# Optimization experiments

Measured on AMD Instinct MI355X. Metric: run time of the kernel, lower is better.

## Reference

```python
import jax, jax.numpy as jnp
import numpy as np

N_DIM = 100_000      # n: primal variables
M_DIM = 200_000      # m: constraints
NNZ_A = 2_000_000    # nnz of A
NNZ_P_HALF = 250_000 # half of symmetric P nnz (mirrored)
CG_ITERS = 50


def _spmv(vals, rows, cols, v, nseg):
    # COO sparse matvec: out[r] += vals * v[cols]
    return jax.ops.segment_sum(vals * v[cols], rows, num_segments=nseg)


def setup_inputs() -> dict:
    key = jax.random.key(0)
    ks = jax.random.split(key, 16)
    n, m = N_DIM, M_DIM
    A_rows = jax.random.randint(ks[0], (NNZ_A,), 0, m, dtype=jnp.int32)
    A_cols = jax.random.randint(ks[1], (NNZ_A,), 0, n, dtype=jnp.int32)
    A_vals = jax.random.normal(ks[2], (NNZ_A,), jnp.float32) * 0.01
    # symmetric P via mirrored COO pattern
    pr = jax.random.randint(ks[3], (NNZ_P_HALF,), 0, n, dtype=jnp.int32)
    pc = jax.random.randint(ks[4], (NNZ_P_HALF,), 0, n, dtype=jnp.int32)
    pv = jax.random.normal(ks[5], (NNZ_P_HALF,), jnp.float32) * 0.01
    P_rows = jnp.concatenate([pr, pc])
    P_cols = jnp.concatenate([pc, pr])
    P_vals = jnp.concatenate([pv, pv])
    q = jax.random.normal(ks[6], (n,), jnp.float32)
    b = jax.random.normal(ks[7], (m,), jnp.float32)
    x = jax.random.normal(ks[8], (n,), jnp.float32)
    y = jnp.maximum(jax.random.normal(ks[9], (m,), jnp.float32), 0.0)
    s = jnp.maximum(jax.random.normal(ks[10], (m,), jnp.float32), 0.0)
    # data perturbations (dP shares P's symmetric pattern, dA shares A's pattern)
    dpv = jax.random.normal(ks[11], (NNZ_P_HALF,), jnp.float32) * 1e-3
    dP_vals = jnp.concatenate([dpv, dpv])
    dA_vals = jax.random.normal(ks[12], (NNZ_A,), jnp.float32) * 1e-3
    dq = jax.random.normal(ks[13], (n,), jnp.float32) * 1e-3
    db = jax.random.normal(ks[14], (m,), jnp.float32) * 1e-3
    return dict(P_rows=P_rows, P_cols=P_cols, P_vals=P_vals,
                A_rows=A_rows, A_cols=A_cols, A_vals=A_vals,
                q=q, b=b, x=x, y=y, s=s,
                dP_vals=dP_vals, dA_vals=dA_vals, dq=dq, db=db)


def reference(P_rows, P_cols, P_vals, A_rows, A_cols, A_vals,
              q, b, x, y, s, dP_vals, dA_vals, dq, db):
    n, m = q.shape[0], b.shape[0]
    Pmv = lambda v: _spmv(P_vals, P_rows, P_cols, v, n)
    Amv = lambda v: _spmv(A_vals, A_rows, A_cols, v, m)
    ATmv = lambda v: _spmv(A_vals, A_cols, A_rows, v, n)
    dPmv = lambda v: _spmv(dP_vals, P_rows, P_cols, v, n)
    dAmv = lambda v: _spmv(dA_vals, A_rows, A_cols, v, m)
    dATmv = lambda v: _spmv(dA_vals, A_cols, A_rows, v, n)

    # cone projection onto K* = R_+^m and its Jacobian (diagonal mask)
    v_ks = y - s
    mask = (v_ks > 0).astype(x.dtype)
    pi_m = jnp.maximum(v_ks, 0.0)     # pi_z = (x, Pi_{K*}(y-s), 1)
    tau = jnp.asarray(1.0, x.dtype)

    Px = Pmv(x)
    xTPx = x @ Px
    c3 = q + 2.0 * Px                  # d/dx of -x^T P x / tau at tau=1 -> -(q + 2Px)

    def Fmv(vv):
        # F = DzQ(pi_z) @ dPi - dPi + I
        vn, vm, vt = vv[:n], vv[n:n + m], vv[-1]
        un, um, ut = vn, mask * vm, vt          # dPi v
        r1 = Pmv(un) + ATmv(um) + q * ut        # [P, A^T, q]
        r2 = -Amv(un) + b * ut                  # [-A, 0, b]
        r3 = -(c3 @ un) - (b @ um) + xTPx * ut  # [-(q+2Px)^T, -b^T, x^TPx]
        return jnp.concatenate([r1 - un + vn, r2 - um + vm, (r3 - ut + vt)[None]])

    def FTmv(ww):
        # F^T = dPi @ (DzQ^T - I) + I   (dPi symmetric diagonal)
        wn, wm, wt = ww[:n], ww[n:n + m], ww[-1]
        t_n = Pmv(wn) - ATmv(wm) - c3 * wt
        t_m = Amv(wn) - b * wt
        t_t = (q @ wn) + (b @ wm) + xTPx * wt
        return jnp.concatenate([t_n, mask * (t_m - wm) + wm, t_t[None]])

    # d_data_Q applied at u = pi_z
    dd_n = dPmv(x) + dATmv(pi_m) + dq * tau
    dd_m = -dAmv(x) + db * tau
    dd_t = -(dq @ x) - (db @ pi_m) - (x @ dPmv(x)) / tau
    dd = jnp.concatenate([dd_n, dd_m, dd_t[None]])

    def solve_case():
        # least-squares solve of F dz = -dd via CG on normal equations (LSMR-equivalent solution)
        normal_op = lambda v: FTmv(Fmv(v))
        rhs = FTmv(-dd)
        dz, _ = jax.scipy.sparse.linalg.cg(normal_op, rhs, tol=1e-8, maxiter=CG_ITERS)
        return dz

    dz = jax.lax.cond(jnp.allclose(dd, 0.0), lambda: jnp.zeros_like(dd), solve_case)

    dzn, dzm, dzt = dz[:n], dz[n:n + m], dz[-1]
    dx = dzn - x * dzt
    t = mask * dzm                     # dPi_{K*}(v) @ dz_m
    dy = t - y * dzt
    ds = t - dzm - s * dzt
    return dx, dy, ds
```

## Files before the change

### kernel.cpp

```cpp
#include <hip/hip_runtime.h>

#define N_DIM 100000
#define M_DIM 200000
#define NNZ_A 2000000
#define NNZ_P 500000
#define NNZ_GN (NNZ_A + NNZ_P)
#define NMSUM 300000
#define NM1   300001
#define CG_ITERS 20
#define TPB 256
#define NSLOT 512
#define GOFF (20 * 5 * 64)
#define SETOFF (GOFF + 21 * 64)
#define REDSZ (SETOFF + 6 * 64)


__device__ __forceinline__ void blk_red_add(double v, double* dst) {
    __shared__ double sb[TPB];
    int tid = threadIdx.x;
    __syncthreads();
    sb[tid] = v;
    __syncthreads();
    for (int sh = TPB / 2; sh > 0; sh >>= 1) {
        if (tid < sh) sb[tid] += sb[tid + sh];
        __syncthreads();
    }
    if (tid == 0) atomicAdd(dst, sb[0]);
}

__device__ __forceinline__ void blk_red_add2(double v1, double v2, double* d1, double* d2) {
    __shared__ double sb1[TPB];
    __shared__ double sb2[TPB];
    int tid = threadIdx.x;
    __syncthreads();
    sb1[tid] = v1; sb2[tid] = v2;
    __syncthreads();
    for (int sh = TPB / 2; sh > 0; sh >>= 1) {
        if (tid < sh) { sb1[tid] += sb1[tid + sh]; sb2[tid] += sb2[tid + sh]; }
        __syncthreads();
    }
    if (tid == 0) { atomicAdd(d1, sb1[0]); atomicAdd(d2, sb2[0]); }
}

__device__ __forceinline__ double blk_sum64w(const double* src) {
    __shared__ double bsh;
    int t = threadIdx.x;
    if (t < 64) {
        double v = src[t];
        v += __shfl_xor(v, 32); v += __shfl_xor(v, 16); v += __shfl_xor(v, 8);
        v += __shfl_xor(v, 4);  v += __shfl_xor(v, 2);  v += __shfl_xor(v, 1);
        if (t == 0) bsh = v;
    }
    __syncthreads();
    double r = bsh;
    __syncthreads();
    return r;
}

__device__ __forceinline__ double row_dotx4(const int4* __restrict__ pp, int b2, int e2,
                                            const double* __restrict__ vin) {
    double s = 0.0;
    int k = b2;
    for (; k + 4 <= e2; k += 4) {
        int4 a = pp[k], b = pp[k + 1], c = pp[k + 2], d = pp[k + 3];
        double g0 = vin[a.x], g1 = vin[a.z], g2 = vin[b.x], g3 = vin[b.z];
        double g4 = vin[c.x], g5 = vin[c.z], g6 = vin[d.x], g7 = vin[d.z];
        s += (double)__int_as_float(a.y) * g0;
        s += (double)__int_as_float(a.w) * g1;
        s += (double)__int_as_float(b.y) * g2;
        s += (double)__int_as_float(b.w) * g3;
        s += (double)__int_as_float(c.y) * g4;
        s += (double)__int_as_float(c.w) * g5;
        s += (double)__int_as_float(d.y) * g6;
        s += (double)__int_as_float(d.w) * g7;
    }
    for (; k < e2; ++k) {
        int4 a = pp[k];
        s += (double)__int_as_float(a.y) * vin[a.x];
        s += (double)__int_as_float(a.w) * vin[a.z];
    }
    return s;
}

__device__ __forceinline__ double row_dotx4_half(const int4* __restrict__ pp, int b2, int e2,
                                                 const double* __restrict__ vin, int half) {
    int len = e2 - b2;
    int h1 = (len + 1) >> 1;
    int kb = b2 + (half ? h1 : 0);
    int ke = half ? e2 : (b2 + h1);
    double s = 0.0;
    int k = kb;
    for (; k + 4 <= ke; k += 4) {
        int4 a = pp[k], b = pp[k + 1], c = pp[k + 2], d = pp[k + 3];
        double g0 = vin[a.x], g1 = vin[a.z], g2 = vin[b.x], g3 = vin[b.z];
        double g4 = vin[c.x], g5 = vin[c.z], g6 = vin[d.x], g7 = vin[d.z];
        s += (double)__int_as_float(a.y) * g0;
        s += (double)__int_as_float(a.w) * g1;
        s += (double)__int_as_float(b.y) * g2;
        s += (double)__int_as_float(b.w) * g3;
        s += (double)__int_as_float(c.y) * g4;
        s += (double)__int_as_float(c.w) * g5;
        s += (double)__int_as_float(d.y) * g6;
        s += (double)__int_as_float(d.w) * g7;
    }
    for (; k + 2 <= ke; k += 2) {
        int4 a = pp[k], b = pp[k + 1];
        double g0 = vin[a.x], g1 = vin[a.z], g2 = vin[b.x], g3 = vin[b.z];
        s += (double)__int_as_float(a.y) * g0;
        s += (double)__int_as_float(a.w) * g1;
        s += (double)__int_as_float(b.y) * g2;
        s += (double)__int_as_float(b.w) * g3;
    }
    if (k < ke) {
        int4 a = pp[k];
        s += (double)__int_as_float(a.y) * vin[a.x];
        s += (double)__int_as_float(a.w) * vin[a.z];
    }
    s += __shfl_xor(s, 1);
    return s;
}

__device__ __forceinline__ double row_dot_d(const int2* __restrict__ pair,
                                            const float* __restrict__ dval, int beg, int end,
                                            const double* __restrict__ vin) {
    double s = 0.0;
    int k = beg;
    for (; k + 4 <= end; k += 4) {
        int c0 = pair[k].x, c1 = pair[k + 1].x, c2 = pair[k + 2].x, c3v = pair[k + 3].x;
        float d0 = dval[k], d1 = dval[k + 1], d2 = dval[k + 2], d3 = dval[k + 3];
        double g0 = vin[c0], g1 = vin[c1], g2 = vin[c2], g3 = vin[c3v];
        s += (double)d0 * g0;
        s += (double)d1 * g1;
        s += (double)d2 * g2;
        s += (double)d3 * g3;
    }
    for (; k < end; ++k)
        s += (double)dval[k] * vin[pair[k].x];
    return s;
}

__global__ __launch_bounds__(TPB) void k_init(double* sc, const float* y, const float* s,
                                              const float* x, double* mask_d, double* xpim,
                                              double* xcg, double* red,
                                              int* nP, int* cntGn, int* cntAr) {
    long i = (long)blockIdx.x * TPB + threadIdx.x;
    if (i < NSLOT) sc[i] = 0.0;
    if (i < REDSZ) red[i] = 0.0;
    if (i < M_DIM) {
        double v = (double)y[i] - (double)s[i];
        mask_d[i] = v > 0.0 ? 1.0 : 0.0;
        xpim[N_DIM + i] = v > 0.0 ? v : 0.0;
        cntAr[i] = 0;
    }
    if (i < N_DIM) {
        xpim[i] = (double)x[i];
        nP[i] = 0; cntGn[i] = 0;
    }
    if (i < NM1) xcg[i] = 0.0;
}

__global__ __launch_bounds__(TPB) void k_hist(const int* Ar, const int* Ac, const int* Pr,
                                              int* nP, int* cntGn, int* cntAr,
                                              int* seqP, int* seqGn, int* seqAr) {
    long k = (long)blockIdx.x * TPB + threadIdx.x;
    if (k < NNZ_A) {
        seqGn[k] = atomicAdd(&cntGn[Ac[k]], 1);
        seqAr[k] = atomicAdd(&cntAr[Ar[k]], 1);
    }
    if (k < NNZ_P) seqP[k] = atomicAdd(&nP[Pr[k]], 1);
}

__global__ __launch_bounds__(TPB) void k_comb(const int* nP, int* cntGn) {
    int i = blockIdx.x * TPB + threadIdx.x;
    if (i < N_DIM) cntGn[i] += nP[i];
}

__global__ __launch_bounds__(TPB) void k_scan1(const int* cnt, int len, int* exc, int* blksum) {
    __shared__ int sb[TPB];
    int i = blockIdx.x * TPB + threadIdx.x;
    int c = (i < len) ? cnt[i] : 0;
    int v = c + (c & 1);
    sb[threadIdx.x] = v;
    __syncthreads();
    for (int sh = 1; sh < TPB; sh <<= 1) {
        int t = (threadIdx.x >= sh) ? sb[threadIdx.x - sh] : 0;
        __syncthreads();
        sb[threadIdx.x] += t;
        __syncthreads();
    }
    if (i < len) exc[i] = sb[threadIdx.x] - v;
    if (threadIdx.x == TPB - 1) blksum[blockIdx.x] = sb[TPB - 1];
}

__global__ __launch_bounds__(1024) void k_scan2(int* blksum, int nb, int* total_out) {
    __shared__ int sb[1024];
    int t = threadIdx.x;
    int v = (t < nb) ? blksum[t] : 0;
    sb[t] = v;
    __syncthreads();
    for (int sh = 1; sh < 1024; sh <<= 1) {
        int x = (t >= sh) ? sb[t - sh] : 0;
        __syncthreads();
        sb[t] += x;
        __syncthreads();
    }
    if (t < nb) blksum[t] = sb[t] - v;
    if (t == nb - 1) *total_out = sb[t];
}

__global__ __launch_bounds__(TPB) void k_scan3(int* exc, const int* blksum, int len) {
    int i = blockIdx.x * TPB + threadIdx.x;
    if (i < len) exc[i] += blksum[blockIdx.x];
}

__global__ __launch_bounds__(TPB) void k_fillGn(const int* Pr, const int* Pc, const float* Pv,
                                                const float* dPv,
                                                const int* Ar, const int* Ac, const float* Av,
                                                const float* dAv,
                                                const int* rptrGn, const int* nP,
                                                const int* seqP, const int* seqGn,
                                                int2* pGn, float* dvalGn) {
    long k = (long)blockIdx.x * TPB + threadIdx.x;
    if (k < NNZ_P) {
        int r0 = Pr[k];
        int pos = rptrGn[r0] + seqP[k];
        pGn[pos] = make_int2(Pc[k], __float_as_int(Pv[k]));
        dvalGn[pos] = dPv[k];
    }
    if (k < NNZ_A) {
        int c0 = Ac[k];
        int pos = rptrGn[c0] + nP[c0] + seqGn[k];
        pGn[pos] = make_int2(N_DIM + Ar[k], __float_as_int(Av[k]));
        dvalGn[pos] = dAv[k];
    }
}
__global__ __launch_bounds__(TPB) void k_fillAr(const int* Ar, const int* Ac, const float* Av,
                                                const float* dAv, const int* rptrAr,
                                                const int* seqAr, int2* pAr, float* dvalAr) {
    long k = (long)blockIdx.x * TPB + threadIdx.x;
    if (k < NNZ_A) {
        int pos = rptrAr[Ar[k]] + seqAr[k];
        pAr[pos] = make_int2(Ac[k], __float_as_int(Av[k]));
        dvalAr[pos] = dAv[k];
    }
}

__global__ __launch_bounds__(TPB) void k_pad(const int* cntGn, const int* rptrGn,
                                             int2* pGn, float* dvalGn,
                                             const int* cntAr, const int* rptrAr,
                                             int2* pAr, float* dvalAr) {
    int i = blockIdx.x * TPB + threadIdx.x;
    if (i < N_DIM) {
        int c = cntGn[i];
        if (c & 1) { int pos = rptrGn[i] + c; pGn[pos] = make_int2(0, 0); dvalGn[pos] = 0.0f; }
    }
    if (i < M_DIM) {
        int c = cntAr[i];
        if (c & 1) { int pos = rptrAr[i] + c; pAr[pos] = make_int2(0, 0); dvalAr[pos] = 0.0f; }
    }
}

__global__ __launch_bounds__(TPB) void k_setup_n(const int* __restrict__ rptrGn,
                                                 const int2* __restrict__ pGn,
                                                 const float* __restrict__ dvalGn,
                                                 const int* __restrict__ nP,
                                                 const double* __restrict__ xpim,
                                                 const float* __restrict__ q,
                                                 const float* __restrict__ dq,
                                                 double* c3, double* dd, double* red) {
    int i = blockIdx.x * TPB + threadIdx.x;
    int slot = blockIdx.x & 63;
    double* S = red + SETOFF;
    double lx = 0.0, l1 = 0.0, l3 = 0.0;
    if (i < N_DIM) {
        int beg = rptrGn[i], end = rptrGn[i + 1];
        int np = nP[i];
        double px = 0.0, dpxv = 0.0, sa = 0.0;
        for (int k = beg; k < end; ++k) {
            int2 e = pGn[k];
            float dv = dvalGn[k];
            double g = xpim[e.x];
            if (k - beg < np) {
                px += (double)__int_as_float(e.y) * g;
                dpxv += (double)dv * g;
            } else {
                sa += (double)dv * g;
            }
        }
        c3[i] = (double)q[i] + 2.0 * px;
        dd[i] = dpxv + sa + (double)dq[i];
        double xi = xpim[i];
        lx = xi * px;
        l1 = (double)dq[i] * xi;
        l3 = xi * dpxv;
    }
    blk_red_add2(lx, l1, S + 0 * 64 + slot, S + 1 * 64 + slot);
    blk_red_add(l3, S + 3 * 64 + slot);
}

__global__ __launch_bounds__(TPB) void k_setup_m(const int* __restrict__ rptrAr,
                                                 const int2* __restrict__ pAr,
                                                 const float* __restrict__ dvalAr,
                                                 const double* __restrict__ xpim,
                                                 const float* __restrict__ db, double* dd,
                                                 double* red) {
    int j = blockIdx.x * TPB + threadIdx.x;
    int slot = blockIdx.x & 63;
    double* S = red + SETOFF;
    double l2 = 0.0;
    if (j < M_DIM) {
        double s = row_dot_d(pAr, dvalAr, rptrAr[j], rptrAr[j + 1], xpim);
        dd[N_DIM + j] = -s + (double)db[j];
        l2 = (double)db[j] * xpim[N_DIM + j];
    }
    blk_red_add(l2, S + 2 * 64 + slot);
}

__global__ __launch_bounds__(TPB) void k_negWC(double* dd, double* WC,
                                               const float* q, const float* b,
                                               double* red, double* sc) {
    long i = (long)blockIdx.x * TPB + threadIdx.x;
    int slot = blockIdx.x & 63;
    double* S = red + SETOFF;
    double l8 = 0.0, l9 = 0.0;
    if (i == NMSUM) {
        double xt = 0.0, s1 = 0.0, s2 = 0.0, s3 = 0.0;
        for (int k = 0; k < 64; ++k) {
            xt += S[k]; s1 += S[64 + k]; s2 += S[128 + k]; s3 += S[192 + k];
        }
        sc[0] = xt;
        dd[NMSUM] = s1 + s2 + s3;
    } else if (i < NM1) {
        double nv = -dd[i];
        dd[i] = nv;
        if (i < N_DIM) {
            WC[i] = nv;
            l8 = (double)q[i] * nv;
        } else {
            WC[i] = -nv;
            l9 = (double)b[i - N_DIM] * nv;
        }
    }
    blk_red_add2(l8, l9, S + 4 * 64 + slot, S + 5 * 64 + slot);
}

__global__ __launch_bounds__(TPB) void k_r(const int* __restrict__ rptrGn, const int2* __restrict__ pGn,
                                           const int* __restrict__ rptrAr, const int2* __restrict__ pAr,
                                           const double* __restrict__ WC, const double* __restrict__ c3,
                                           const double* __restrict__ mask_d, const float* __restrict__ b,
                                           const double* __restrict__ dd, double* r, double* p,
                                           double* red, const double* sc) {
    const int4* pGn4 = (const int4*)pGn;
    const int4* pAr4 = (const int4*)pAr;
    long i = (long)blockIdx.x * TPB + threadIdx.x;
    int slot = blockIdx.x & 63;
    double* S = red + SETOFF;
    double* gslot = red + GOFF;
    double rv = 0.0;
    bool wr = false;
    if (i < N_DIM) {
        double s = row_dotx4(pGn4, rptrGn[i] >> 1, rptrGn[i + 1] >> 1, WC);
        rv = s - c3[i] * dd[NMSUM];
        wr = true;
    } else if (i < NMSUM) {
        int j = (int)(i - N_DIM);
        double s = row_dotx4(pAr4, rptrAr[j] >> 1, rptrAr[j + 1] >> 1, WC);
        double wt = dd[NMSUM];
        double tmv = s - (double)b[j] * wt;
        double wm = dd[i];
        rv = mask_d[j] * (tmv - wm) + wm;
        wr = true;
    } else if (i == NMSUM) {
        double e1 = 0.0, e2 = 0.0;
        for (int k = 0; k < 64; ++k) { e1 += S[4 * 64 + k]; e2 += S[5 * 64 + k]; }
        rv = e1 + e2 + sc[0] * dd[NMSUM];
        wr = true;
    }
    double l = 0.0;
    if (wr) { r[i] = rv; p[i] = rv; l = rv * rv; }
    blk_red_add(l, gslot + slot);
}

__global__ __launch_bounds__(TPB) void k_iterA(const double* r, double* p,
                                               const double* mask_d, const double* c3,
                                               const float* b, double* pum,
                                               double* red, double* sc, int it) {
    double* ds = red + (long)it * 5 * 64;
    double* gslot = red + GOFF;
    double gn = blk_sum64w(gslot + (long)it * 64);
    if (blockIdx.x == 0 && threadIdx.x == 0) sc[64 + it] = gn;
    double beta = 0.0;
    if (it > 0) beta = gn / sc[64 + it - 1];
    long i = (long)blockIdx.x * TPB + threadIdx.x;
    int slot = blockIdx.x & 63;
    double l1 = 0.0, l2 = 0.0;
    if (i < NM1) {
        double pn;
        if (it > 0) {
            pn = r[i] + beta * p[i];
            p[i] = pn;
        } else {
            pn = p[i];
        }
        if (i < N_DIM) {
            l1 = c3[i] * pn;
            pum[i] = pn;
        } else if (i < NMSUM) {
            int j = (int)(i - N_DIM);
            double u = mask_d[j] * pn;
            pum[i] = u;
            l2 = (double)b[j] * u;
        }
    }
    blk_red_add2(l1, l2, ds + 0 * 64 + slot, ds + 1 * 64 + slot);
}

__global__ __launch_bounds__(TPB) void k_fmv(const int* __restrict__ rptrGn, const int2* __restrict__ pGn,
                                             const int* __restrict__ rptrAr, const int2* __restrict__ pAr,
                                             const float* __restrict__ q, const float* __restrict__ b,
                                             const double* __restrict__ p, const double* __restrict__ pum,
                                             double* __restrict__ Fpc, double* sc, double* red, int it) {
    const int4* pGn4 = (const int4*)pGn;
    const int4* pAr4 = (const int4*)pAr;
    double* ds = red + (long)it * 5 * 64;
    long t = (long)blockIdx.x * TPB + threadIdx.x;
    long i = t >> 1;
    int half = (int)(t & 1);
    int slot = blockIdx.x & 63;
    double ut = p[NMSUM];
    double l1 = 0.0, l2 = 0.0;
    if (i < N_DIM) {
        int ii = (int)i;
        double s = row_dotx4_half(pGn4, rptrGn[ii] >> 1, rptrGn[ii + 1] >> 1, pum, half);
        if (half == 0) {
            double r1 = s + (double)q[ii] * ut;
            double v = (r1 - p[i]) + p[i];
            Fpc[i] = v;
            l1 = (double)q[ii] * v;
        }
    } else if (i < NMSUM) {
        int j = (int)(i - N_DIM);
        double s = row_dotx4_half(pAr4, rptrAr[j] >> 1, rptrAr[j + 1] >> 1, pum, half);
        if (half == 0) {
            double r2 = -s + (double)b[j] * ut;
            double v = (r2 - pum[i]) + p[i];
            Fpc[i] = -v;
            l2 = (double)b[j] * v;
        }
    }
    blk_red_add2(l1, l2, ds + 2 * 64 + slot, ds + 3 * 64 + slot);
    if (blockIdx.x == gridDim.x - 1) {
        double d1 = blk_sum64w(ds + 0 * 64);
        double d2 = blk_sum64w(ds + 1 * 64);
        if (threadIdx.x == 0) {
            double r3 = -d1 - d2 + sc[0] * ut;
            sc[16 + it] = (r3 - ut) + ut;
        }
    }
}

__global__ __launch_bounds__(TPB) void k_ftmv(const int* __restrict__ rptrGn, const int2* __restrict__ pGn,
                                              const int* __restrict__ rptrAr, const int2* __restrict__ pAr,
                                              const float* __restrict__ b, const double* __restrict__ mask_d,
                                              const double* __restrict__ c3,
                                              const double* __restrict__ Fpc, const double* __restrict__ p,
                                              double* __restrict__ Ap, double* sc, double* red, int it) {
    const int4* pGn4 = (const int4*)pGn;
    const int4* pAr4 = (const int4*)pAr;
    double* ds = red + (long)it * 5 * 64;
    long t = (long)blockIdx.x * TPB + threadIdx.x;
    long i = t >> 1;
    int half = (int)(t & 1);
    int slot = blockIdx.x & 63;
    double wt = sc[16 + it];
    double l = 0.0;
    if (i < N_DIM) {
        int ii = (int)i;
        double s = row_dotx4_half(pGn4, rptrGn[ii] >> 1, rptrGn[ii + 1] >> 1, Fpc, half);
        if (half == 0) {
            double v = s - c3[ii] * wt;
            Ap[i] = v;
            l = p[i] * v;
        }
    } else if (i < NMSUM) {
        int j = (int)(i - N_DIM);
        double s = row_dotx4_half(pAr4, rptrAr[j] >> 1, rptrAr[j + 1] >> 1, Fpc, half);
        if (half == 0) {
            double tmv = s - (double)b[j] * wt;
            double wm = -Fpc[i];
            double v = mask_d[j] * (tmv - wm) + wm;
            Ap[i] = v;
            l = p[i] * v;
        }
    }
    blk_red_add(l, ds + 4 * 64 + slot);
    if (blockIdx.x == gridDim.x - 1) {
        double e1 = blk_sum64w(ds + 2 * 64);
        double e2 = blk_sum64w(ds + 3 * 64);
        if (threadIdx.x == 0) {
            double tt = e1 + e2 + sc[0] * wt;
            Ap[NMSUM] = tt;
            atomicAdd(ds + 4 * 64 + slot, p[NMSUM] * tt);
        }
    }
}

__global__ __launch_bounds__(TPB) void k_upd(const double* p, const double* Ap,
                                             double* xcg, double* r, double* red,
                                             const double* sc, int it) {
    double* ds = red + (long)it * 5 * 64;
    double* gslot = red + GOFF;
    double gcur = sc[64 + it];
    double pq = blk_sum64w(ds + 4 * 64);
    double alpha = gcur / pq;
    long i = (long)blockIdx.x * TPB + threadIdx.x;
    int slot = blockIdx.x & 63;
    double l = 0.0;
    if (i < NM1) {
        xcg[i] += alpha * p[i];
        double rn = r[i] - alpha * Ap[i];
        r[i] = rn;
        l = rn * rn;
    }
    blk_red_add(l, gslot + (long)(it + 1) * 64 + slot);
}

__global__ __launch_bounds__(TPB) void k_final(const double* xcg, const double* mask_d,
                                               const float* x, const float* y, const float* s,
                                               float* out) {
    int i = blockIdx.x * TPB + threadIdx.x;
    double dzt = xcg[NMSUM];
    if (i < N_DIM) {
        out[i] = (float)(xcg[i] - (double)x[i] * dzt);
    } else if (i < NMSUM) {
        int j = i - N_DIM;
        double dzm = xcg[N_DIM + j];
        double t = mask_d[j] * dzm;
        out[N_DIM + j] = (float)(t - (double)y[j] * dzt);
        out[N_DIM + M_DIM + j] = (float)(t - dzm - (double)s[j] * dzt);
    }
}

extern "C" void kernel_launch(void* const* d_in, const int* in_sizes, int n_in,
                              void* d_out, int out_size, void* d_ws, size_t ws_size,
                              hipStream_t stream) {
    const int*   Pr  = (const int*)d_in[0];
    const int*   Pc  = (const int*)d_in[1];
    const float* Pv  = (const float*)d_in[2];
    const int*   Ar  = (const int*)d_in[3];
    const int*   Ac  = (const int*)d_in[4];
    const float* Av  = (const float*)d_in[5];
    const float* q   = (const float*)d_in[6];
    const float* b   = (const float*)d_in[7];
    const float* x   = (const float*)d_in[8];
    const float* yv  = (const float*)d_in[9];
    const float* sv  = (const float*)d_in[10];
    const float* dPv = (const float*)d_in[11];
    const float* dAv = (const float*)d_in[12];
    const float* dq  = (const float*)d_in[13];
    const float* db  = (const float*)d_in[14];
    float* out = (float*)d_out;

    char* wp = (char*)d_ws;
    auto alloc = [&](size_t bytes) { char* r0 = wp; wp += (bytes + 255) & ~255ull; return r0; };

    double* sc     = (double*)alloc(NSLOT * 8);
    double* red    = (double*)alloc((size_t)REDSZ * 8);
    double* mask_d = (double*)alloc((size_t)M_DIM * 8);
    double* xpim   = (double*)alloc((size_t)NMSUM * 8);
    double* c3     = (double*)alloc((size_t)N_DIM * 8);
    double* dd     = (double*)alloc((size_t)NM1 * 8);
    double* r      = (double*)alloc((size_t)NM1 * 8);
    double* p      = (double*)alloc((size_t)NM1 * 8);
    double* xcg    = (double*)alloc((size_t)NM1 * 8);
    double* Ap     = (double*)alloc((size_t)NM1 * 8);
    double* pum    = (double*)alloc((size_t)NMSUM * 8);
    double* Fpc    = (double*)alloc((size_t)NMSUM * 8);
    double* WC     = (double*)alloc((size_t)NMSUM * 8);
    int2*  pGn    = (int2*)alloc(((size_t)NNZ_GN + N_DIM) * 8);
    int2*  pAr    = (int2*)alloc(((size_t)NNZ_A + M_DIM) * 8);
    float* dvalGn = (float*)alloc(((size_t)NNZ_GN + N_DIM) * 4);
    float* dvalAr = (float*)alloc(((size_t)NNZ_A + M_DIM) * 4);
    int*   rptrGn = (int*)alloc((size_t)(N_DIM + 1) * 4);
    int*   rptrAr = (int*)alloc((size_t)(M_DIM + 1) * 4);
    int*   nP     = (int*)alloc((size_t)N_DIM * 4);
    int*   cntGn  = (int*)alloc((size_t)N_DIM * 4);
    int*   cntAr  = (int*)alloc((size_t)M_DIM * 4);
    int*   seqP   = (int*)alloc((size_t)NNZ_P * 4);
    int*   seqGn  = (int*)alloc((size_t)NNZ_A * 4);
    int*   seqAr  = (int*)alloc((size_t)NNZ_A * 4);
    int*   blks   = (int*)alloc(1024 * 4);

    auto g = [](long n) { return dim3((unsigned)((n + TPB - 1) / TPB)); };
    dim3 gs((unsigned)((2L * NM1 + TPB - 1) / TPB + 1));

    hipLaunchKernelGGL(k_init, g(NM1), dim3(TPB), 0, stream, sc, yv, sv, x, mask_d, xpim, xcg, red,
                       nP, cntGn, cntAr);
    hipLaunchKernelGGL(k_hist, g(NNZ_A), dim3(TPB), 0, stream, Ar, Ac, Pr, nP, cntGn, cntAr,
                       seqP, seqGn, seqAr);
    hipLaunchKernelGGL(k_comb, g(N_DIM), dim3(TPB), 0, stream, nP, cntGn);

    auto scan = [&](int* cnt, int len, int* rptr) {
        int nb = (len + TPB - 1) / TPB;
        hipLaunchKernelGGL(k_scan1, dim3((unsigned)nb), dim3(TPB), 0, stream, cnt, len, rptr, blks);
        hipLaunchKernelGGL(k_scan2, dim3(1), dim3(1024), 0, stream, blks, nb, rptr + len);
        hipLaunchKernelGGL(k_scan3, dim3((unsigned)nb), dim3(TPB), 0, stream, rptr, blks, len);
    };
    scan(cntGn, N_DIM, rptrGn);
    scan(cntAr, M_DIM, rptrAr);

    hipLaunchKernelGGL(k_fillGn, g(NNZ_A), dim3(TPB), 0, stream, Pr, Pc, Pv, dPv,
                       Ar, Ac, Av, dAv, rptrGn, nP, seqP, seqGn, pGn, dvalGn);
    hipLaunchKernelGGL(k_fillAr, g(NNZ_A), dim3(TPB), 0, stream, Ar, Ac, Av, dAv,
                       rptrAr, seqAr, pAr, dvalAr);
    hipLaunchKernelGGL(k_pad, g(M_DIM), dim3(TPB), 0, stream, cntGn, rptrGn, pGn, dvalGn,
                       cntAr, rptrAr, pAr, dvalAr);

    hipLaunchKernelGGL(k_setup_n, g(N_DIM), dim3(TPB), 0, stream, rptrGn, pGn, dvalGn, nP,
                       xpim, q, dq, c3, dd, red);
    hipLaunchKernelGGL(k_setup_m, g(M_DIM), dim3(TPB), 0, stream, rptrAr, pAr, dvalAr, xpim, db, dd, red);
    hipLaunchKernelGGL(k_negWC, g(NM1), dim3(TPB), 0, stream, dd, WC, q, b, red, sc);
    hipLaunchKernelGGL(k_r, g(NM1), dim3(TPB), 0, stream, rptrGn, pGn, rptrAr, pAr,
                       WC, c3, mask_d, b, dd, r, p, red, sc);

    for (int it = 0; it < CG_ITERS; ++it) {
        hipLaunchKernelGGL(k_iterA, g(NM1), dim3(TPB), 0, stream, r, p, mask_d, c3, b, pum, red, sc, it);
        hipLaunchKernelGGL(k_fmv,   gs, dim3(TPB), 0, stream, rptrGn, pGn, rptrAr, pAr,
                           q, b, p, pum, Fpc, sc, red, it);
        hipLaunchKernelGGL(k_ftmv,  gs, dim3(TPB), 0, stream, rptrGn, pGn, rptrAr, pAr,
                           b, mask_d, c3, Fpc, p, Ap, sc, red, it);
        hipLaunchKernelGGL(k_upd,   g(NM1), dim3(TPB), 0, stream, p, Ap, xcg, r, red, sc, it);
    }

    hipLaunchKernelGGL(k_final, g(NMSUM), dim3(TPB), 0, stream, xcg, mask_d, x, yv, sv, out);
}
```

Measured before the change: 2.124 ms.

## Split long Gn rows across four lanes and fuse setup/scan kernels

The forward and transposed matvecs now give each Gn row (the P plus A-transpose columns, about 25 entries on average) to four threads instead of two, and combine the partial sums with two xor shuffles. The A rows keep two threads each. The setup phase also merges the two per-vector scans into single launches, folds the pad step into the fill step and fuses the n/m setup kernels, which cuts launch count and serialization. In exchange the grid is larger and more threads sit idle on short rows. The histogram stores become nontemporal.

```diff
diff --git a/kernel.cpp b/kernel.cpp
--- a/kernel.cpp
+++ b/kernel.cpp
@@ -13,6 +13,8 @@
 #define GOFF (20 * 5 * 64)
 #define SETOFF (GOFF + 21 * 64)
 #define REDSZ (SETOFF + 6 * 64)
+#define GN_BLKS ((N_DIM + TPB - 1) / TPB)
+#define AR_BLKS ((M_DIM + TPB - 1) / TPB)
 
 
 __device__ __forceinline__ void blk_red_add(double v, double* dst) {
@@ -82,12 +84,8 @@
     return s;
 }
 
-__device__ __forceinline__ double row_dotx4_half(const int4* __restrict__ pp, int b2, int e2,
-                                                 const double* __restrict__ vin, int half) {
-    int len = e2 - b2;
-    int h1 = (len + 1) >> 1;
-    int kb = b2 + (half ? h1 : 0);
-    int ke = half ? e2 : (b2 + h1);
+__device__ __forceinline__ double chunk_dot(const int4* __restrict__ pp, int kb, int ke,
+                                            const double* __restrict__ vin) {
     double s = 0.0;
     int k = kb;
     for (; k + 4 <= ke; k += 4) {
@@ -116,7 +114,31 @@
         s += (double)__int_as_float(a.y) * vin[a.x];
         s += (double)__int_as_float(a.w) * vin[a.z];
     }
+    return s;
+}
+
+__device__ __forceinline__ double row_dotx4_half(const int4* __restrict__ pp, int b2, int e2,
+                                                 const double* __restrict__ vin, int half) {
+    int len = e2 - b2;
+    int h1 = (len + 1) >> 1;
+    int kb = b2 + (half ? h1 : 0);
+    int ke = half ? e2 : (b2 + h1);
+    double s = chunk_dot(pp, kb, ke, vin);
     s += __shfl_xor(s, 1);
+    return s;
+}
+
+__device__ __forceinline__ double row_dotx4_quarter(const int4* __restrict__ pp, int b2, int e2,
+                                                    const double* __restrict__ vin, int qd) {
+    int len = e2 - b2;
+    int h = (len + 3) >> 2;
+    int kb = b2 + qd * h;
+    int ke = kb + h;
+    if (kb > e2) kb = e2;
+    if (ke > e2) ke = e2;
+    double s = chunk_dot(pp, kb, ke, vin);
+    s += __shfl_xor(s, 1);
+    s += __shfl_xor(s, 2);
     return s;
 }
 
@@ -164,38 +186,52 @@
                                               int* seqP, int* seqGn, int* seqAr) {
     long k = (long)blockIdx.x * TPB + threadIdx.x;
     if (k < NNZ_A) {
-        seqGn[k] = atomicAdd(&cntGn[Ac[k]], 1);
-        seqAr[k] = atomicAdd(&cntAr[Ar[k]], 1);
-    }
-    if (k < NNZ_P) seqP[k] = atomicAdd(&nP[Pr[k]], 1);
-}
-
-__global__ __launch_bounds__(TPB) void k_comb(const int* nP, int* cntGn) {
-    int i = blockIdx.x * TPB + threadIdx.x;
-    if (i < N_DIM) cntGn[i] += nP[i];
-}
-
-__global__ __launch_bounds__(TPB) void k_scan1(const int* cnt, int len, int* exc, int* blksum) {
+        int sg = atomicAdd(&cntGn[Ac[k]], 1);
+        int sa = atomicAdd(&cntAr[Ar[k]], 1);
+        __builtin_nontemporal_store(sg, &seqGn[k]);
+        __builtin_nontemporal_store(sa, &seqAr[k]);
+    }
+    if (k < NNZ_P) {
+        int sp = atomicAdd(&nP[Pr[k]], 1);
+        __builtin_nontemporal_store(sp, &seqP[k]);
+    }
+}
+
+__global__ __launch_bounds__(TPB) void k_scan1b(const int* nP, int* cntGn, const int* cntAr,
+                                                int* rptrGn, int* rptrAr, int* blksum) {
     __shared__ int sb[TPB];
-    int i = blockIdx.x * TPB + threadIdx.x;
-    int c = (i < len) ? cnt[i] : 0;
+    int bid = blockIdx.x;
+    int t = threadIdx.x;
+    int c = 0;
+    int i;
+    bool isGn = bid < GN_BLKS;
+    if (isGn) {
+        i = bid * TPB + t;
+        if (i < N_DIM) { c = cntGn[i] + nP[i]; cntGn[i] = c; }
+    } else {
+        i = (bid - GN_BLKS) * TPB + t;
+        if (i < M_DIM) c = cntAr[i];
+    }
     int v = c + (c & 1);
-    sb[threadIdx.x] = v;
+    sb[t] = v;
     __syncthreads();
     for (int sh = 1; sh < TPB; sh <<= 1) {
-        int t = (threadIdx.x >= sh) ? sb[threadIdx.x - sh] : 0;
+        int u = (t >= sh) ? sb[t - sh] : 0;
         __syncthreads();
-        sb[threadIdx.x] += t;
+        sb[t] += u;
         __syncthreads();
     }
-    if (i < len) exc[i] = sb[threadIdx.x] - v;
-    if (threadIdx.x == TPB - 1) blksum[blockIdx.x] = sb[TPB - 1];
-}
-
-__global__ __launch_bounds__(1024) void k_scan2(int* blksum, int nb, int* total_out) {
+    if (isGn) { if (i < N_DIM) rptrGn[i] = sb[t] - v; }
+    else      { if (i < M_DIM) rptrAr[i] = sb[t] - v; }
+    if (t == TPB - 1) blksum[bid] = sb[TPB - 1];
+}
+
+__global__ __launch_bounds__(1024) void k_scan2b(int* blksum, int* rptrGn, int* rptrAr) {
     __shared__ int sb[1024];
     int t = threadIdx.x;
-    int v = (t < nb) ? blksum[t] : 0;
+    int base = (blockIdx.x == 0) ? 0 : GN_BLKS;
+    int nb = (blockIdx.x == 0) ? GN_BLKS : AR_BLKS;
+    int v = (t < nb) ? blksum[base + t] : 0;
     sb[t] = v;
     __syncthreads();
     for (int sh = 1; sh < 1024; sh <<= 1) {
@@ -204,13 +240,23 @@
         sb[t] += x;
         __syncthreads();
     }
-    if (t < nb) blksum[t] = sb[t] - v;
-    if (t == nb - 1) *total_out = sb[t];
-}
-
-__global__ __launch_bounds__(TPB) void k_scan3(int* exc, const int* blksum, int len) {
-    int i = blockIdx.x * TPB + threadIdx.x;
-    if (i < len) exc[i] += blksum[blockIdx.x];
+    if (t < nb) blksum[base + t] = sb[t] - v;
+    if (t == nb - 1) {
+        if (blockIdx.x == 0) rptrGn[N_DIM] = sb[t];
+        else                 rptrAr[M_DIM] = sb[t];
+    }
+}
+
+__global__ __launch_bounds__(TPB) void k_scan3b(int* rptrGn, int* rptrAr, const int* blksum) {
+    int bid = blockIdx.x;
+    int t = threadIdx.x;
+    if (bid < GN_BLKS) {
+        int i = bid * TPB + t;
+        if (i < N_DIM) rptrGn[i] += blksum[bid];
+    } else {
+        int i = (bid - GN_BLKS) * TPB + t;
+        if (i < M_DIM) rptrAr[i] += blksum[bid];
+    }
 }
 
 __global__ __launch_bounds__(TPB) void k_fillGn(const int* Pr, const int* Pc, const float* Pv,
@@ -234,44 +280,44 @@
         dvalGn[pos] = dAv[k];
     }
 }
-__global__ __launch_bounds__(TPB) void k_fillAr(const int* Ar, const int* Ac, const float* Av,
-                                                const float* dAv, const int* rptrAr,
-                                                const int* seqAr, int2* pAr, float* dvalAr) {
+
+__global__ __launch_bounds__(TPB) void k_fillArPad(const int* Ar, const int* Ac, const float* Av,
+                                                   const float* dAv, const int* rptrAr,
+                                                   const int* seqAr, int2* pAr, float* dvalAr,
+                                                   const int* cntGn, const int* rptrGn,
+                                                   int2* pGn, float* dvalGn, const int* cntAr) {
     long k = (long)blockIdx.x * TPB + threadIdx.x;
     if (k < NNZ_A) {
         int pos = rptrAr[Ar[k]] + seqAr[k];
         pAr[pos] = make_int2(Ac[k], __float_as_int(Av[k]));
         dvalAr[pos] = dAv[k];
     }
-}
-
-__global__ __launch_bounds__(TPB) void k_pad(const int* cntGn, const int* rptrGn,
-                                             int2* pGn, float* dvalGn,
-                                             const int* cntAr, const int* rptrAr,
-                                             int2* pAr, float* dvalAr) {
-    int i = blockIdx.x * TPB + threadIdx.x;
-    if (i < N_DIM) {
-        int c = cntGn[i];
-        if (c & 1) { int pos = rptrGn[i] + c; pGn[pos] = make_int2(0, 0); dvalGn[pos] = 0.0f; }
-    }
-    if (i < M_DIM) {
-        int c = cntAr[i];
-        if (c & 1) { int pos = rptrAr[i] + c; pAr[pos] = make_int2(0, 0); dvalAr[pos] = 0.0f; }
-    }
-}
-
-__global__ __launch_bounds__(TPB) void k_setup_n(const int* __restrict__ rptrGn,
-                                                 const int2* __restrict__ pGn,
-                                                 const float* __restrict__ dvalGn,
-                                                 const int* __restrict__ nP,
-                                                 const double* __restrict__ xpim,
-                                                 const float* __restrict__ q,
-                                                 const float* __restrict__ dq,
-                                                 double* c3, double* dd, double* red) {
+    if (k < N_DIM) {
+        int c = cntGn[k];
+        if (c & 1) { int pos = rptrGn[k] + c; pGn[pos] = make_int2(0, 0); dvalGn[pos] = 0.0f; }
+    }
+    if (k < M_DIM) {
+        int c = cntAr[k];
+        if (c & 1) { int pos = rptrAr[k] + c; pAr[pos] = make_int2(0, 0); dvalAr[pos] = 0.0f; }
+    }
+}
+
+__global__ __launch_bounds__(TPB) void k_setup(const int* __restrict__ rptrGn,
+                                               const int2* __restrict__ pGn,
+                                               const float* __restrict__ dvalGn,
+                                               const int* __restrict__ nP,
+                                               const int* __restrict__ rptrAr,
+                                               const int2* __restrict__ pAr,
+                                               const float* __restrict__ dvalAr,
+                                               const double* __restrict__ xpim,
+                                               const float* __restrict__ q,
+                                               const float* __restrict__ dq,
+                                               const float* __restrict__ db,
+                                               double* c3, double* dd, double* red) {
     int i = blockIdx.x * TPB + threadIdx.x;
     int slot = blockIdx.x & 63;
     double* S = red + SETOFF;
-    double lx = 0.0, l1 = 0.0, l3 = 0.0;
+    double lx = 0.0, l1 = 0.0, l2 = 0.0, l3 = 0.0;
     if (i < N_DIM) {
         int beg = rptrGn[i], end = rptrGn[i + 1];
         int np = nP[i];
@@ -294,26 +340,13 @@
         l1 = (double)dq[i] * xi;
         l3 = xi * dpxv;
     }
+    if (i < M_DIM) {
+        double s = row_dot_d(pAr, dvalAr, rptrAr[i], rptrAr[i + 1], xpim);
+        dd[N_DIM + i] = -s + (double)db[i];
+        l2 = (double)db[i] * xpim[N_DIM + i];
+    }
     blk_red_add2(lx, l1, S + 0 * 64 + slot, S + 1 * 64 + slot);
-    blk_red_add(l3, S + 3 * 64 + slot);
-}
-
-__global__ __launch_bounds__(TPB) void k_setup_m(const int* __restrict__ rptrAr,
-                                                 const int2* __restrict__ pAr,
-                                                 const float* __restrict__ dvalAr,
-                                                 const double* __restrict__ xpim,
-                                                 const float* __restrict__ db, double* dd,
-                                                 double* red) {
-    int j = blockIdx.x * TPB + threadIdx.x;
-    int slot = blockIdx.x & 63;
-    double* S = red + SETOFF;
-    double l2 = 0.0;
-    if (j < M_DIM) {
-        double s = row_dot_d(pAr, dvalAr, rptrAr[j], rptrAr[j + 1], xpim);
-        dd[N_DIM + j] = -s + (double)db[j];
-        l2 = (double)db[j] * xpim[N_DIM + j];
-    }
-    blk_red_add(l2, S + 2 * 64 + slot);
+    blk_red_add2(l3, l2, S + 3 * 64 + slot, S + 2 * 64 + slot);
 }
 
 __global__ __launch_bounds__(TPB) void k_negWC(double* dd, double* WC,
@@ -424,27 +457,29 @@
     const int4* pAr4 = (const int4*)pAr;
     double* ds = red + (long)it * 5 * 64;
     long t = (long)blockIdx.x * TPB + threadIdx.x;
-    long i = t >> 1;
-    int half = (int)(t & 1);
     int slot = blockIdx.x & 63;
     double ut = p[NMSUM];
     double l1 = 0.0, l2 = 0.0;
-    if (i < N_DIM) {
-        int ii = (int)i;
-        double s = row_dotx4_half(pGn4, rptrGn[ii] >> 1, rptrGn[ii + 1] >> 1, pum, half);
-        if (half == 0) {
-            double r1 = s + (double)q[ii] * ut;
+    if (t < 4L * N_DIM) {
+        int i = (int)(t >> 2);
+        int qd = (int)(t & 3);
+        double s = row_dotx4_quarter(pGn4, rptrGn[i] >> 1, rptrGn[i + 1] >> 1, pum, qd);
+        if (qd == 0) {
+            double r1 = s + (double)q[i] * ut;
             double v = (r1 - p[i]) + p[i];
             Fpc[i] = v;
-            l1 = (double)q[ii] * v;
-        }
-    } else if (i < NMSUM) {
-        int j = (int)(i - N_DIM);
+            l1 = (double)q[i] * v;
+        }
+    } else if (t < 4L * N_DIM + 2L * M_DIM) {
+        long u = t - 4L * N_DIM;
+        int j = (int)(u >> 1);
+        int half = (int)(u & 1);
+        int gj = N_DIM + j;
         double s = row_dotx4_half(pAr4, rptrAr[j] >> 1, rptrAr[j + 1] >> 1, pum, half);
         if (half == 0) {
             double r2 = -s + (double)b[j] * ut;
-            double v = (r2 - pum[i]) + p[i];
-            Fpc[i] = -v;
+            double v = (r2 - pum[gj]) + p[gj];
+            Fpc[gj] = -v;
             l2 = (double)b[j] * v;
         }
     }
@@ -469,28 +504,30 @@
     const int4* pAr4 = (const int4*)pAr;
     double* ds = red + (long)it * 5 * 64;
     long t = (long)blockIdx.x * TPB + threadIdx.x;
-    long i = t >> 1;
-    int half = (int)(t & 1);
     int slot = blockIdx.x & 63;
     double wt = sc[16 + it];
     double l = 0.0;
-    if (i < N_DIM) {
-        int ii = (int)i;
-        double s = row_dotx4_half(pGn4, rptrGn[ii] >> 1, rptrGn[ii + 1] >> 1, Fpc, half);
-        if (half == 0) {
-            double v = s - c3[ii] * wt;
+    if (t < 4L * N_DIM) {
+        int i = (int)(t >> 2);
+        int qd = (int)(t & 3);
+        double s = row_dotx4_quarter(pGn4, rptrGn[i] >> 1, rptrGn[i + 1] >> 1, Fpc, qd);
+        if (qd == 0) {
+            double v = s - c3[i] * wt;
             Ap[i] = v;
             l = p[i] * v;
         }
-    } else if (i < NMSUM) {
-        int j = (int)(i - N_DIM);
+    } else if (t < 4L * N_DIM + 2L * M_DIM) {
+        long u = t - 4L * N_DIM;
+        int j = (int)(u >> 1);
+        int half = (int)(u & 1);
+        int gj = N_DIM + j;
         double s = row_dotx4_half(pAr4, rptrAr[j] >> 1, rptrAr[j + 1] >> 1, Fpc, half);
         if (half == 0) {
             double tmv = s - (double)b[j] * wt;
-            double wm = -Fpc[i];
+            double wm = -Fpc[gj];
             double v = mask_d[j] * (tmv - wm) + wm;
-            Ap[i] = v;
-            l = p[i] * v;
+            Ap[gj] = v;
+            l = p[gj] * v;
         }
     }
     blk_red_add(l, ds + 4 * 64 + slot);
@@ -589,36 +626,27 @@
     int*   seqP   = (int*)alloc((size_t)NNZ_P * 4);
     int*   seqGn  = (int*)alloc((size_t)NNZ_A * 4);
     int*   seqAr  = (int*)alloc((size_t)NNZ_A * 4);
-    int*   blks   = (int*)alloc(1024 * 4);
+    int*   blks   = (int*)alloc(2048 * 4);
 
     auto g = [](long n) { return dim3((unsigned)((n + TPB - 1) / TPB)); };
-    dim3 gs((unsigned)((2L * NM1 + TPB - 1) / TPB + 1));
+    dim3 gs((unsigned)((4L * N_DIM + 2L * M_DIM) / TPB + 1));
+    dim3 gscan((unsigned)(GN_BLKS + AR_BLKS));
 
     hipLaunchKernelGGL(k_init, g(NM1), dim3(TPB), 0, stream, sc, yv, sv, x, mask_d, xpim, xcg, red,
                        nP, cntGn, cntAr);
     hipLaunchKernelGGL(k_hist, g(NNZ_A), dim3(TPB), 0, stream, Ar, Ac, Pr, nP, cntGn, cntAr,
                        seqP, seqGn, seqAr);
-    hipLaunchKernelGGL(k_comb, g(N_DIM), dim3(TPB), 0, stream, nP, cntGn);
-
-    auto scan = [&](int* cnt, int len, int* rptr) {
-        int nb = (len + TPB - 1) / TPB;
-        hipLaunchKernelGGL(k_scan1, dim3((unsigned)nb), dim3(TPB), 0, stream, cnt, len, rptr, blks);
-        hipLaunchKernelGGL(k_scan2, dim3(1), dim3(1024), 0, stream, blks, nb, rptr + len);
-        hipLaunchKernelGGL(k_scan3, dim3((unsigned)nb), dim3(TPB), 0, stream, rptr, blks, len);
-    };
-    scan(cntGn, N_DIM, rptrGn);
-    scan(cntAr, M_DIM, rptrAr);
+    hipLaunchKernelGGL(k_scan1b, gscan, dim3(TPB), 0, stream, nP, cntGn, cntAr, rptrGn, rptrAr, blks);
+    hipLaunchKernelGGL(k_scan2b, dim3(2), dim3(1024), 0, stream, blks, rptrGn, rptrAr);
+    hipLaunchKernelGGL(k_scan3b, gscan, dim3(TPB), 0, stream, rptrGn, rptrAr, blks);
 
     hipLaunchKernelGGL(k_fillGn, g(NNZ_A), dim3(TPB), 0, stream, Pr, Pc, Pv, dPv,
                        Ar, Ac, Av, dAv, rptrGn, nP, seqP, seqGn, pGn, dvalGn);
-    hipLaunchKernelGGL(k_fillAr, g(NNZ_A), dim3(TPB), 0, stream, Ar, Ac, Av, dAv,
-                       rptrAr, seqAr, pAr, dvalAr);
-    hipLaunchKernelGGL(k_pad, g(M_DIM), dim3(TPB), 0, stream, cntGn, rptrGn, pGn, dvalGn,
-                       cntAr, rptrAr, pAr, dvalAr);
-
-    hipLaunchKernelGGL(k_setup_n, g(N_DIM), dim3(TPB), 0, stream, rptrGn, pGn, dvalGn, nP,
-                       xpim, q, dq, c3, dd, red);
-    hipLaunchKernelGGL(k_setup_m, g(M_DIM), dim3(TPB), 0, stream, rptrAr, pAr, dvalAr, xpim, db, dd, red);
+    hipLaunchKernelGGL(k_fillArPad, g(NNZ_A), dim3(TPB), 0, stream, Ar, Ac, Av, dAv,
+                       rptrAr, seqAr, pAr, dvalAr, cntGn, rptrGn, pGn, dvalGn, cntAr);
+
+    hipLaunchKernelGGL(k_setup, g(M_DIM), dim3(TPB), 0, stream, rptrGn, pGn, dvalGn, nP,
+                       rptrAr, pAr, dvalAr, xpim, q, dq, db, c3, dd, red);
     hipLaunchKernelGGL(k_negWC, g(NM1), dim3(TPB), 0, stream, dd, WC, q, b, red, sc);
     hipLaunchKernelGGL(k_r, g(NM1), dim3(TPB), 0, stream, rptrGn, pGn, rptrAr, pAr,
                        WC, c3, mask_d, b, dd, r, p, red, sc);
```

Measured after the change: 2.140 ms. Within noise of the previous version (+0.7%).
